# Performance work log

Measured on AMD Instinct MI355X. Metric: run time of the kernel, lower is better.

The kernel has to match this reference:

```python
import jax, jax.numpy as jnp
import numpy as np

BS, N, D, H = 4, 2048, 512, 8
DK = D // H
XAVIER_STD = float(np.sqrt(2.0 / (D + D)))  # xavier_normal_, gain=1


def setup_inputs() -> dict:
    key = jax.random.key(0)
    ks = jax.random.split(key, 10)
    Q = jax.random.normal(ks[0], (BS, N, D), jnp.float32)
    K = jax.random.normal(ks[1], (BS, N, D), jnp.float32)
    V = jax.random.normal(ks[2], (BS, N, D), jnp.float32)
    q_mas = jax.random.randint(ks[3], (BS, N, 1), 0, 2).astype(jnp.float32)
    k_mas = jax.random.randint(ks[4], (BS, N, 1), 0, 2).astype(jnp.float32)
    # 0/1 attention mask; force self-edges so no row is fully masked (avoids NaN softmax)
    att_mas = jax.random.randint(ks[5], (BS, N, N), 0, 2).astype(jnp.float32)
    att_mas = jnp.maximum(att_mas, jnp.eye(N, dtype=jnp.float32)[None])
    WQ = jax.random.normal(ks[6], (D, D), jnp.float32) * XAVIER_STD
    WK = jax.random.normal(ks[7], (D, D), jnp.float32) * XAVIER_STD
    WV = jax.random.normal(ks[8], (D, D), jnp.float32) * XAVIER_STD
    WO = jax.random.normal(ks[9], (D, D), jnp.float32) * XAVIER_STD
    return {"Q": Q, "K": K, "V": V, "q_mas": q_mas, "k_mas": k_mas,
            "att_mas": att_mas, "WQ": WQ, "WK": WK, "WV": WV, "WO": WO}


def reference(Q, K, V, q_mas, k_mas, att_mas, WQ, WK, WV, WO):
    bs, n, d = Q.shape
    h, dk = H, DK
    qm = q_mas.reshape(bs, 1, n, 1)  # (bs,1,n,1)
    km = k_mas.reshape(bs, 1, n, 1)
    # nn.Linear (no bias): x @ W.T ; split heads -> (bs,h,n,dk); apply pre-masks
    Qh = qm * (Q @ WQ.T).reshape(bs, n, h, dk).transpose(0, 2, 1, 3)
    Kh = km * (K @ WK.T).reshape(bs, n, h, dk).transpose(0, 2, 1, 3)
    Vh = km * (V @ WV.T).reshape(bs, n, h, dk).transpose(0, 2, 1, 3)
    scores = jnp.einsum('bhqd,bhkd->bhqk', Qh, Kh) / jnp.sqrt(jnp.float32(dk))
    mas = att_mas.reshape(bs, 1, n, n)
    scores = jnp.where(mas.astype(bool), scores, -jnp.inf)
    attn = jax.nn.softmax(scores, axis=-1) * mas
    y = jnp.einsum('bhqk,bhkd->bhqd', attn, Vh) * km  # post-mask (note: km over query dim, as in source)
    y = y.transpose(0, 2, 1, 3).reshape(bs, n, d)
    y = (y @ WO.T) * k_mas.reshape(bs, n, 1)
    return y
```

## Files before the change

kernel.cpp:

```cpp
#include <hip/hip_runtime.h>


#define BS_    4
#define NSEQ   2048
#define DMODEL 512
#define NH     8
#define DKH    64
#define MROWS  (BS_ * NSEQ)
#define NW32   (NSEQ / 32)

typedef unsigned short ushort_t;
typedef __attribute__((ext_vector_type(8))) short short8;
typedef __attribute__((ext_vector_type(4))) float floatx4;

__device__ __forceinline__ ushort_t f2bf(float f) {
    unsigned int x = __builtin_bit_cast(unsigned int, f);
    unsigned int lsb = (x >> 16) & 1u;
    x += 0x7fffu + lsb;
    return (ushort_t)(x >> 16);
}
__device__ __forceinline__ floatx4 mfma_bf16(short8 a, short8 b, floatx4 c) {
    return __builtin_amdgcn_mfma_f32_16x16x32_bf16(a, b, c, 0, 0, 0);
}
__device__ __forceinline__ void gld16(const ushort_t* g, ushort_t* l) {
    __builtin_amdgcn_global_load_lds(
        (const __attribute__((address_space(1))) unsigned int*)g,
        (__attribute__((address_space(3))) unsigned int*)l, 16, 0, 0);
}
__device__ __forceinline__ unsigned int cvt_pk_bf16(float lo, float hi) {
    unsigned int r;
    asm("v_cvt_pk_bf16_f32 %0, %1, %2" : "=v"(r) : "v"(lo), "v"(hi));
    return r;
}

__global__ __launch_bounds__(256) void cvt3_kernel(const float* __restrict__ a,
                                                   const float* __restrict__ b,
                                                   const float* __restrict__ c,
                                                   ushort_t* __restrict__ dst, int n4) {
    const float* src = (blockIdx.y == 0) ? a : (blockIdx.y == 1) ? b : c;
    ushort_t* d = dst + (size_t)blockIdx.y * ((size_t)n4 * 4);
    const int i = blockIdx.x * blockDim.x + threadIdx.x;
    const float4 v = ((const float4*)src)[i];
    ushort4 o;
    o.x = f2bf(v.x); o.y = f2bf(v.y); o.z = f2bf(v.z); o.w = f2bf(v.w);
    ((ushort4*)d)[i] = o;
}

__global__ __launch_bounds__(256) void cvt4_kernel(const float* __restrict__ a,
                                                   const float* __restrict__ b,
                                                   const float* __restrict__ c,
                                                   const float* __restrict__ e,
                                                   ushort_t* __restrict__ dst, int n4) {
    const float* src = (blockIdx.y == 0) ? a : (blockIdx.y == 1) ? b
                     : (blockIdx.y == 2) ? c : e;
    ushort_t* d = dst + (size_t)blockIdx.y * ((size_t)n4 * 4);
    const int i = blockIdx.x * blockDim.x + threadIdx.x;
    const float4 v = ((const float4*)src)[i];
    ushort4 o;
    o.x = f2bf(v.x); o.y = f2bf(v.y); o.z = f2bf(v.z); o.w = f2bf(v.w);
    ((ushort4*)d)[i] = o;
}

__global__ __launch_bounds__(256) void mask_pack(const float* __restrict__ am,
                                                 unsigned int* __restrict__ mb) {
    const int t = blockIdx.x * 256 + threadIdx.x;
    const float4* src = (const float4*)am + (size_t)t * 8;
    unsigned int m = 0;
#pragma unroll
    for (int j = 0; j < 8; ++j) {
        const float4 v = src[j];
        m |= (v.x != 0.f ? 1u : 0u) << (4 * j);
        m |= (v.y != 0.f ? 1u : 0u) << (4 * j + 1);
        m |= (v.z != 0.f ? 1u : 0u) << (4 * j + 2);
        m |= (v.w != 0.f ? 1u : 0u) << (4 * j + 3);
    }
    mb[t] = m;
}

__global__ __launch_bounds__(256) void gemm_proj(const ushort_t* __restrict__ Xall,
                                                 const ushort_t* __restrict__ Wall,
                                                 const float* __restrict__ qmas,
                                                 const float* __restrict__ kmas,
                                                 ushort_t* __restrict__ Qh,
                                                 ushort_t* __restrict__ Kh,
                                                 ushort_t* __restrict__ Vt) {
    __shared__ ushort_t As[128 * 32];
    __shared__ ushort_t Bs[128 * 32];
    const int z = blockIdx.z;
    const ushort_t* X  = Xall + (size_t)z * MROWS * DMODEL;
    const ushort_t* Wb = Wall + (size_t)z * DMODEL * DMODEL;
    const float* rowmask = (z == 0) ? qmas : kmas;

    const int tid  = threadIdx.x;
    const int wave = tid >> 6;
    const int lane = tid & 63;
    const int l16  = lane & 15;
    const int quad = lane >> 4;
    const int wr   = wave >> 1;
    const int wc   = wave & 1;
    const int m0   = blockIdx.x * 128;
    const int n0   = blockIdx.y * 128;
    const int crow = lane >> 2;
    const int koff = (lane & 3) * 8;

    floatx4 acc[4][4];
#pragma unroll
    for (int t = 0; t < 4; ++t)
#pragma unroll
        for (int u = 0; u < 4; ++u) acc[t][u] = (floatx4){0.f, 0.f, 0.f, 0.f};

    for (int k0 = 0; k0 < DMODEL; k0 += 32) {
#pragma unroll
        for (int c2 = 0; c2 < 2; ++c2) {
            const int c = wave * 2 + c2;
            gld16(X  + (size_t)(m0 + c * 16 + crow) * DMODEL + k0 + koff, &As[c * 512]);
            gld16(Wb + (size_t)(n0 + c * 16 + crow) * DMODEL + k0 + koff, &Bs[c * 512]);
        }
        __syncthreads();
        short8 a[4], b[4];
#pragma unroll
        for (int t = 0; t < 4; ++t)
            a[t] = *(const short8*)&As[(wr * 64 + t * 16 + l16) * 32 + quad * 8];
#pragma unroll
        for (int u = 0; u < 4; ++u)
            b[u] = *(const short8*)&Bs[(wc * 64 + u * 16 + l16) * 32 + quad * 8];
#pragma unroll
        for (int t = 0; t < 4; ++t)
#pragma unroll
            for (int u = 0; u < 4; ++u) acc[t][u] = mfma_bf16(a[t], b[u], acc[t][u]);
        __syncthreads();
    }

    float rm[4][4];
#pragma unroll
    for (int t = 0; t < 4; ++t)
#pragma unroll
        for (int r = 0; r < 4; ++r)
            rm[t][r] = rowmask[m0 + wr * 64 + t * 16 + quad * 4 + r];
    if (z == 0) {
#pragma unroll
        for (int t = 0; t < 4; ++t)
#pragma unroll
            for (int r = 0; r < 4; ++r) rm[t][r] *= 0.18033688011112042f;
    }

    const int bb    = m0 >> 11;
    const int nbase = (m0 & (NSEQ - 1)) + wr * 64;
#pragma unroll
    for (int t = 0; t < 4; ++t) {
#pragma unroll
        for (int u = 0; u < 4; ++u) {
            const int d = n0 + wc * 64 + u * 16 + l16;
            const int h = d >> 6, cc = d & 63;
            if (z < 2) {
                ushort_t* dst = (z == 0) ? Qh : Kh;
#pragma unroll
                for (int r = 0; r < 4; ++r) {
                    const int n = nbase + t * 16 + quad * 4 + r;
                    dst[((size_t)(bb * NH + h) * NSEQ + n) * DKH + cc] =
                        f2bf(acc[t][u][r] * rm[t][r]);
                }
            } else {
                ushort4 pk;
                pk.x = f2bf(acc[t][u][0] * rm[t][0]);
                pk.y = f2bf(acc[t][u][1] * rm[t][1]);
                pk.z = f2bf(acc[t][u][2] * rm[t][2]);
                pk.w = f2bf(acc[t][u][3] * rm[t][3]);
                const int n = nbase + t * 16 + quad * 4;
                *(ushort4*)(Vt + ((size_t)(bb * NH + h) * DKH + cc) * NSEQ + n) = pk;
            }
        }
    }
}

__global__ __launch_bounds__(256) void gemm_out(const ushort_t* __restrict__ X,
                                                const ushort_t* __restrict__ Wb,
                                                const float* __restrict__ rowmask,
                                                float* __restrict__ dst) {
    __shared__ ushort_t As[128 * 32];
    __shared__ ushort_t Bs[128 * 32];
    const int tid  = threadIdx.x;
    const int wave = tid >> 6;
    const int lane = tid & 63;
    const int l16  = lane & 15;
    const int quad = lane >> 4;
    const int wr   = wave >> 1;
    const int wc   = wave & 1;
    const int m0   = blockIdx.x * 128;
    const int n0   = blockIdx.y * 128;
    const int crow = lane >> 2;
    const int koff = (lane & 3) * 8;

    floatx4 acc[4][4];
#pragma unroll
    for (int t = 0; t < 4; ++t)
#pragma unroll
        for (int u = 0; u < 4; ++u) acc[t][u] = (floatx4){0.f, 0.f, 0.f, 0.f};

    for (int k0 = 0; k0 < DMODEL; k0 += 32) {
#pragma unroll
        for (int c2 = 0; c2 < 2; ++c2) {
            const int c = wave * 2 + c2;
            gld16(X  + (size_t)(m0 + c * 16 + crow) * DMODEL + k0 + koff, &As[c * 512]);
            gld16(Wb + (size_t)(n0 + c * 16 + crow) * DMODEL + k0 + koff, &Bs[c * 512]);
        }
        __syncthreads();
        short8 a[4], b[4];
#pragma unroll
        for (int t = 0; t < 4; ++t)
            a[t] = *(const short8*)&As[(wr * 64 + t * 16 + l16) * 32 + quad * 8];
#pragma unroll
        for (int u = 0; u < 4; ++u)
            b[u] = *(const short8*)&Bs[(wc * 64 + u * 16 + l16) * 32 + quad * 8];
#pragma unroll
        for (int t = 0; t < 4; ++t)
#pragma unroll
            for (int u = 0; u < 4; ++u) acc[t][u] = mfma_bf16(a[t], b[u], acc[t][u]);
        __syncthreads();
    }

#pragma unroll
    for (int t = 0; t < 4; ++t) {
#pragma unroll
        for (int r = 0; r < 4; ++r) {
            const int m = m0 + wr * 64 + t * 16 + quad * 4 + r;
            const float rm = rowmask[m];
#pragma unroll
            for (int u = 0; u < 4; ++u) {
                const int d = n0 + wc * 64 + u * 16 + l16;
                dst[(size_t)m * DMODEL + d] = acc[t][u][r] * rm;
            }
        }
    }
}

__global__ __launch_bounds__(256) void attn_kernel(const ushort_t* __restrict__ Qh,
                                                   const ushort_t* __restrict__ Kh,
                                                   const ushort_t* __restrict__ Vt,
                                                   const unsigned int* __restrict__ Mb,
                                                   const float* __restrict__ kmas,
                                                   ushort_t* __restrict__ y) {
    __shared__ __align__(16) ushort_t Ks[128 * 72];
    __shared__ __align__(16) ushort_t Vs[64 * 136];
    __shared__ __align__(16) ushort_t Ps[4][16 * 136];

    const int tid  = threadIdx.x;
    const int wave = tid >> 6;
    const int lane = tid & 63;
    const int l16  = lane & 15;
    const int quad = lane >> 4;
    const int h    = blockIdx.y;
    const int b    = blockIdx.z;
    const int qw   = blockIdx.x * 64 + wave * 16;

    const ushort_t* Kb = Kh + (size_t)(b * NH + h) * NSEQ * DKH;
    const ushort_t* Vb = Vt + (size_t)(b * NH + h) * DKH * NSEQ;
    const unsigned int* Mrow = Mb + ((size_t)(b * NSEQ + qw) + l16) * NW32;

    const ushort_t* Qp = Qh + ((size_t)((b * NH + h) * NSEQ) + qw + l16) * DKH + quad * 8;
    const short8 qfa = *(const short8*)Qp;
    const short8 qfb = *(const short8*)(Qp + 32);

    float lpart = 0.f;
    floatx4 accO[4];
#pragma unroll
    for (int ct = 0; ct < 4; ++ct) accO[ct] = (floatx4){0.f, 0.f, 0.f, 0.f};

    for (int kt = 0; kt < NSEQ / 128; ++kt) {
        const int k0 = kt * 128;

        short8 kv[4], vv[4];
#pragma unroll
        for (int i = 0; i < 4; ++i) {
            const int c = tid + i * 256;
            kv[i] = *(const short8*)(Kb + (size_t)(k0 + (c >> 3)) * DKH + (c & 7) * 8);
        }
#pragma unroll
        for (int i = 0; i < 4; ++i) {
            const int c = tid + i * 256;
            vv[i] = *(const short8*)(Vb + (size_t)(c >> 4) * NSEQ + k0 + (c & 15) * 8);
        }
        const uint4 mw = *(const uint4*)(Mrow + (k0 >> 5));

        __syncthreads();
#pragma unroll
        for (int i = 0; i < 4; ++i) {
            const int c = tid + i * 256;
            *(short8*)&Ks[(c >> 3) * 72 + (c & 7) * 8] = kv[i];
        }
#pragma unroll
        for (int i = 0; i < 4; ++i) {
            const int c = tid + i * 256;
            *(short8*)&Vs[(c >> 4) * 136 + (c & 15) * 8] = vv[i];
        }
        __syncthreads();

        floatx4 S[8];
#pragma unroll
        for (int fr = 0; fr < 8; ++fr) {
            const short8 ka = *(const short8*)&Ks[(fr * 16 + l16) * 72 + quad * 8];
            const short8 kb = *(const short8*)&Ks[(fr * 16 + l16) * 72 + 32 + quad * 8];
            floatx4 s = {0.f, 0.f, 0.f, 0.f};
            s = mfma_bf16(ka, qfa, s);
            s = mfma_bf16(kb, qfb, s);
            S[fr] = s;
        }

        const unsigned int wsh[4] = {mw.x >> (quad * 4), mw.y >> (quad * 4),
                                     mw.z >> (quad * 4), mw.w >> (quad * 4)};
#pragma unroll
        for (int fr = 0; fr < 8; ++fr) {
            float p[4];
#pragma unroll
            for (int r = 0; r < 4; ++r) {
                const int bitp = ((fr & 1) << 4) + r;
                const unsigned int mm =
                    (unsigned int)((int)(wsh[fr >> 1] << (31 - bitp)) >> 31);
                const float e = exp2f(S[fr][r]);
                const unsigned int pb = __builtin_bit_cast(unsigned int, e) & mm;
                p[r] = __builtin_bit_cast(float, pb);
                lpart += p[r];
            }
            uint2 pk;
            pk.x = cvt_pk_bf16(p[0], p[1]);
            pk.y = cvt_pk_bf16(p[2], p[3]);
            *(uint2*)&Ps[wave][l16 * 136 + fr * 16 + quad * 4] = pk;
        }

        __builtin_amdgcn_wave_barrier();
        short8 pf[4];
#pragma unroll
        for (int kf = 0; kf < 4; ++kf)
            pf[kf] = *(const short8*)&Ps[wave][l16 * 136 + kf * 32 + quad * 8];
        __builtin_amdgcn_wave_barrier();

#pragma unroll
        for (int ct = 0; ct < 4; ++ct) {
#pragma unroll
            for (int kf = 0; kf < 4; ++kf) {
                const short8 vb = *(const short8*)&Vs[(ct * 16 + l16) * 136 + kf * 32 + quad * 8];
                accO[ct] = mfma_bf16(pf[kf], vb, accO[ct]);
            }
        }
    }

    float lfull = lpart;
    lfull += __shfl_xor(lfull, 16);
    lfull += __shfl_xor(lfull, 32);
#pragma unroll
    for (int r = 0; r < 4; ++r) {
        const int q = qw + quad * 4 + r;
        const float l = __shfl(lfull, quad * 4 + r);
        const float scale = kmas[b * NSEQ + q] / l;
#pragma unroll
        for (int ct = 0; ct < 4; ++ct) {
            y[(size_t)(b * NSEQ + q) * DMODEL + h * DKH + ct * 16 + l16] =
                f2bf(accO[ct][r] * scale);
        }
    }
}

extern "C" void kernel_launch(void* const* d_in, const int* in_sizes, int n_in,
                              void* d_out, int out_size, void* d_ws, size_t ws_size,
                              hipStream_t stream) {
    (void)in_sizes; (void)n_in; (void)out_size; (void)ws_size;
    const float* Q  = (const float*)d_in[0];
    const float* K  = (const float*)d_in[1];
    const float* V  = (const float*)d_in[2];
    const float* qm = (const float*)d_in[3];
    const float* km = (const float*)d_in[4];
    const float* am = (const float*)d_in[5];
    const float* WQ = (const float*)d_in[6];
    const float* WK = (const float*)d_in[7];
    const float* WV = (const float*)d_in[8];
    const float* WO = (const float*)d_in[9];

    const size_t XN = (size_t)MROWS * DMODEL;
    const size_t WN = (size_t)DMODEL * DMODEL;
    ushort_t* Xbf = (ushort_t*)d_ws;
    ushort_t* Wbf = Xbf + 3 * XN;
    ushort_t* WOb = Wbf + 3 * WN;
    ushort_t* Qh  = Wbf + 4 * WN;
    ushort_t* Kh  = Qh + XN;
    ushort_t* Vt  = Kh + XN;
    ushort_t* y   = Vt + XN;
    unsigned int* Mbits = (unsigned int*)Xbf;
    float* out = (float*)d_out;

    hipLaunchKernelGGL(cvt3_kernel, dim3(4096, 3), dim3(256), 0, stream,
                       Q, K, V, Xbf, (int)(XN / 4));
    hipLaunchKernelGGL(cvt4_kernel, dim3(256, 4), dim3(256), 0, stream,
                       WQ, WK, WV, WO, Wbf, (int)(WN / 4));

    hipLaunchKernelGGL(gemm_proj, dim3(MROWS / 128, DMODEL / 128, 3), dim3(256), 0, stream,
                       Xbf, Wbf, qm, km, Qh, Kh, Vt);

    hipLaunchKernelGGL(mask_pack, dim3((BS_ * NSEQ * NSEQ / 32) / 256), dim3(256), 0, stream,
                       am, Mbits);

    hipLaunchKernelGGL(attn_kernel, dim3(NSEQ / 64, NH, BS_), dim3(256), 0, stream,
                       Qh, Kh, Vt, Mbits, km, y);

    hipLaunchKernelGGL(gemm_out, dim3(MROWS / 128, DMODEL / 128), dim3(256), 0, stream,
                       y, WOb, km, out);
}
```

Baseline: 292.8 us.

## Prefetch next K/V tile in registers, alias P into K LDS, fuse mask packing

The attention loop now loads the next 128-key K/V tile and its mask words into registers while the current tile is computed, so global load latency overlaps the MFMA and softmax work. The per-wave P staging buffer now reuses the K shared-memory tile instead of its own array, guarded by an extra block barrier, and launch bounds ask for 4 blocks per CU. Mask bit-packing is folded into the input-conversion kernel as an extra grid slice writing to the output buffer, removing one launch. The costs are an extra __syncthreads per iteration, more live registers, and half-idle blocks in the mask slice.

```diff
diff --git a/kernel.cpp b/kernel.cpp
--- a/kernel.cpp
+++ b/kernel.cpp
@@ -8,6 +8,7 @@
 #define DKH    64
 #define MROWS  (BS_ * NSEQ)
 #define NW32   (NSEQ / 32)
+#define NWORDS (BS_ * NSEQ * NSEQ / 32)
 
 typedef unsigned short ushort_t;
 typedef __attribute__((ext_vector_type(8))) short short8;
@@ -36,10 +37,28 @@
 __global__ __launch_bounds__(256) void cvt3_kernel(const float* __restrict__ a,
                                                    const float* __restrict__ b,
                                                    const float* __restrict__ c,
-                                                   ushort_t* __restrict__ dst, int n4) {
+                                                   const float* __restrict__ am,
+                                                   ushort_t* __restrict__ dst,
+                                                   unsigned int* __restrict__ mb, int n4) {
+    const int i = blockIdx.x * blockDim.x + threadIdx.x;
+    if (blockIdx.y == 3) {
+        if (i < NWORDS) {
+            const float4* src = (const float4*)am + (size_t)i * 8;
+            unsigned int m = 0;
+#pragma unroll
+            for (int j = 0; j < 8; ++j) {
+                const float4 v = src[j];
+                m |= (v.x != 0.f ? 1u : 0u) << (4 * j);
+                m |= (v.y != 0.f ? 1u : 0u) << (4 * j + 1);
+                m |= (v.z != 0.f ? 1u : 0u) << (4 * j + 2);
+                m |= (v.w != 0.f ? 1u : 0u) << (4 * j + 3);
+            }
+            mb[i] = m;
+        }
+        return;
+    }
     const float* src = (blockIdx.y == 0) ? a : (blockIdx.y == 1) ? b : c;
     ushort_t* d = dst + (size_t)blockIdx.y * ((size_t)n4 * 4);
-    const int i = blockIdx.x * blockDim.x + threadIdx.x;
     const float4 v = ((const float4*)src)[i];
     ushort4 o;
     o.x = f2bf(v.x); o.y = f2bf(v.y); o.z = f2bf(v.z); o.w = f2bf(v.w);
@@ -59,22 +78,6 @@
     ushort4 o;
     o.x = f2bf(v.x); o.y = f2bf(v.y); o.z = f2bf(v.z); o.w = f2bf(v.w);
     ((ushort4*)d)[i] = o;
-}
-
-__global__ __launch_bounds__(256) void mask_pack(const float* __restrict__ am,
-                                                 unsigned int* __restrict__ mb) {
-    const int t = blockIdx.x * 256 + threadIdx.x;
-    const float4* src = (const float4*)am + (size_t)t * 8;
-    unsigned int m = 0;
-#pragma unroll
-    for (int j = 0; j < 8; ++j) {
-        const float4 v = src[j];
-        m |= (v.x != 0.f ? 1u : 0u) << (4 * j);
-        m |= (v.y != 0.f ? 1u : 0u) << (4 * j + 1);
-        m |= (v.z != 0.f ? 1u : 0u) << (4 * j + 2);
-        m |= (v.w != 0.f ? 1u : 0u) << (4 * j + 3);
-    }
-    mb[t] = m;
 }
 
 __global__ __launch_bounds__(256) void gemm_proj(const ushort_t* __restrict__ Xall,
@@ -234,15 +237,14 @@
     }
 }
 
-__global__ __launch_bounds__(256) void attn_kernel(const ushort_t* __restrict__ Qh,
-                                                   const ushort_t* __restrict__ Kh,
-                                                   const ushort_t* __restrict__ Vt,
-                                                   const unsigned int* __restrict__ Mb,
-                                                   const float* __restrict__ kmas,
-                                                   ushort_t* __restrict__ y) {
+__global__ __launch_bounds__(256, 4) void attn_kernel(const ushort_t* __restrict__ Qh,
+                                                      const ushort_t* __restrict__ Kh,
+                                                      const ushort_t* __restrict__ Vt,
+                                                      const unsigned int* __restrict__ Mb,
+                                                      const float* __restrict__ kmas,
+                                                      ushort_t* __restrict__ y) {
     __shared__ __align__(16) ushort_t Ks[128 * 72];
     __shared__ __align__(16) ushort_t Vs[64 * 136];
-    __shared__ __align__(16) ushort_t Ps[4][16 * 136];
 
     const int tid  = threadIdx.x;
     const int wave = tid >> 6;
@@ -253,9 +255,11 @@
     const int b    = blockIdx.z;
     const int qw   = blockIdx.x * 64 + wave * 16;
 
+    ushort_t* Psw = Ks + wave * (16 * 136);
+
     const ushort_t* Kb = Kh + (size_t)(b * NH + h) * NSEQ * DKH;
     const ushort_t* Vb = Vt + (size_t)(b * NH + h) * DKH * NSEQ;
-    const unsigned int* Mrow = Mb + ((size_t)(b * NSEQ + qw) + l16) * NW32;
+    const uint4* Mv = (const uint4*)(Mb + ((size_t)(b * NSEQ + qw) + l16) * NW32);
 
     const ushort_t* Qp = Qh + ((size_t)((b * NH + h) * NSEQ) + qw + l16) * DKH + quad * 8;
     const short8 qfa = *(const short8*)Qp;
@@ -266,21 +270,23 @@
 #pragma unroll
     for (int ct = 0; ct < 4; ++ct) accO[ct] = (floatx4){0.f, 0.f, 0.f, 0.f};
 
+    short8 kv[4], vv[4];
+    uint4 mwn;
+#pragma unroll
+    for (int i = 0; i < 4; ++i) {
+        const int c = tid + i * 256;
+        kv[i] = *(const short8*)(Kb + (size_t)(c >> 3) * DKH + (c & 7) * 8);
+    }
+#pragma unroll
+    for (int i = 0; i < 4; ++i) {
+        const int c = tid + i * 256;
+        vv[i] = *(const short8*)(Vb + (size_t)(c >> 4) * NSEQ + (c & 15) * 8);
+    }
+    mwn = Mv[0];
+
     for (int kt = 0; kt < NSEQ / 128; ++kt) {
         const int k0 = kt * 128;
-
-        short8 kv[4], vv[4];
-#pragma unroll
-        for (int i = 0; i < 4; ++i) {
-            const int c = tid + i * 256;
-            kv[i] = *(const short8*)(Kb + (size_t)(k0 + (c >> 3)) * DKH + (c & 7) * 8);
-        }
-#pragma unroll
-        for (int i = 0; i < 4; ++i) {
-            const int c = tid + i * 256;
-            vv[i] = *(const short8*)(Vb + (size_t)(c >> 4) * NSEQ + k0 + (c & 15) * 8);
-        }
-        const uint4 mw = *(const uint4*)(Mrow + (k0 >> 5));
+        const uint4 mw = mwn;
 
         __syncthreads();
 #pragma unroll
@@ -294,6 +300,21 @@
             *(short8*)&Vs[(c >> 4) * 136 + (c & 15) * 8] = vv[i];
         }
         __syncthreads();
+
+        if (kt + 1 < NSEQ / 128) {
+            const int kn = k0 + 128;
+#pragma unroll
+            for (int i = 0; i < 4; ++i) {
+                const int c = tid + i * 256;
+                kv[i] = *(const short8*)(Kb + (size_t)(kn + (c >> 3)) * DKH + (c & 7) * 8);
+            }
+#pragma unroll
+            for (int i = 0; i < 4; ++i) {
+                const int c = tid + i * 256;
+                vv[i] = *(const short8*)(Vb + (size_t)(c >> 4) * NSEQ + kn + (c & 15) * 8);
+            }
+            mwn = Mv[kt + 1];
+        }
 
         floatx4 S[8];
 #pragma unroll
@@ -305,6 +326,7 @@
             s = mfma_bf16(kb, qfb, s);
             S[fr] = s;
         }
+        __syncthreads();
 
         const unsigned int wsh[4] = {mw.x >> (quad * 4), mw.y >> (quad * 4),
                                      mw.z >> (quad * 4), mw.w >> (quad * 4)};
@@ -315,7 +337,7 @@
             for (int r = 0; r < 4; ++r) {
                 const int bitp = ((fr & 1) << 4) + r;
                 const unsigned int mm =
-                    (unsigned int)((int)(wsh[fr >> 1] << (31 - bitp)) >> 31);
+                    (unsigned int)__builtin_amdgcn_sbfe((int)wsh[fr >> 1], bitp, 1);
                 const float e = exp2f(S[fr][r]);
                 const unsigned int pb = __builtin_bit_cast(unsigned int, e) & mm;
                 p[r] = __builtin_bit_cast(float, pb);
@@ -324,14 +346,14 @@
             uint2 pk;
             pk.x = cvt_pk_bf16(p[0], p[1]);
             pk.y = cvt_pk_bf16(p[2], p[3]);
-            *(uint2*)&Ps[wave][l16 * 136 + fr * 16 + quad * 4] = pk;
+            *(uint2*)&Psw[l16 * 136 + fr * 16 + quad * 4] = pk;
         }
 
         __builtin_amdgcn_wave_barrier();
         short8 pf[4];
 #pragma unroll
         for (int kf = 0; kf < 4; ++kf)
-            pf[kf] = *(const short8*)&Ps[wave][l16 * 136 + kf * 32 + quad * 8];
+            pf[kf] = *(const short8*)&Psw[l16 * 136 + kf * 32 + quad * 8];
         __builtin_amdgcn_wave_barrier();
 
 #pragma unroll
@@ -384,20 +406,17 @@
     ushort_t* Kh  = Qh + XN;
     ushort_t* Vt  = Kh + XN;
     ushort_t* y   = Vt + XN;
-    unsigned int* Mbits = (unsigned int*)Xbf;
+    unsigned int* Mbits = (unsigned int*)d_out;
     float* out = (float*)d_out;
 
-    hipLaunchKernelGGL(cvt3_kernel, dim3(4096, 3), dim3(256), 0, stream,
-                       Q, K, V, Xbf, (int)(XN / 4));
+    hipLaunchKernelGGL(cvt3_kernel, dim3(4096, 4), dim3(256), 0, stream,
+                       Q, K, V, am, Xbf, Mbits, (int)(XN / 4));
     hipLaunchKernelGGL(cvt4_kernel, dim3(256, 4), dim3(256), 0, stream,
                        WQ, WK, WV, WO, Wbf, (int)(WN / 4));
 
     hipLaunchKernelGGL(gemm_proj, dim3(MROWS / 128, DMODEL / 128, 3), dim3(256), 0, stream,
                        Xbf, Wbf, qm, km, Qh, Kh, Vt);
 
-    hipLaunchKernelGGL(mask_pack, dim3((BS_ * NSEQ * NSEQ / 32) / 256), dim3(256), 0, stream,
-                       am, Mbits);
-
     hipLaunchKernelGGL(attn_kernel, dim3(NSEQ / 64, NH, BS_), dim3(256), 0, stream,
                        Qh, Kh, Vt, Mbits, km, y);
 
```

New measurement: 297.5 us. No clear change (+1.6%).
